# Optimization experiments

Hardware: AMD Instinct MI355X
Metric: run time of the kernel (lower is better)

## Reference

```python
import jax, jax.numpy as jnp
import numpy as np

V, PV, D, H, NC = 100000, 50, 128, 128, 2
L, B = 512, 64


def setup_inputs() -> dict:
    key = jax.random.key(0)
    ks = jax.random.split(key, 20)
    s = 0.05
    x = jax.random.randint(ks[0], (L, B), 0, V)
    y = jax.random.randint(ks[1], (B,), 0, 2)
    p = jax.random.randint(ks[2], (L, B), 0, PV)
    # pack_padded_sequence requires descending lengths
    lengths = jnp.sort(jax.random.randint(ks[3], (B,), 1, L + 1))[::-1]
    idx = jnp.arange(L, dtype=jnp.int32)
    left_child = jnp.broadcast_to(idx - 1, (B, L))  # left-deep chain; -1 => no child
    right_child = jnp.full((B, L), -1, dtype=jnp.int32)
    return dict(
        x=x, y=y, p=p, lengths=lengths,
        left_child=left_child, right_child=right_child,
        embed=jax.random.normal(ks[4], (V, D)) * s,
        Wih_f=jax.random.normal(ks[5], (4 * H, D)) * s,
        Whh_f=jax.random.normal(ks[6], (4 * H, H)) * s,
        b_f=jnp.zeros((4 * H,)),
        Wih_b=jax.random.normal(ks[7], (4 * H, D)) * s,
        Whh_b=jax.random.normal(ks[8], (4 * H, H)) * s,
        b_b=jnp.zeros((4 * H,)),
        Wiou=jax.random.normal(ks[9], (D, 3 * H)) * s,
        Uiou=jax.random.normal(ks[10], (H, 3 * H)) * s,
        biou=jnp.zeros((3 * H,)),
        Wf=jax.random.normal(ks[11], (D, H)) * s,
        Uf=jax.random.normal(ks[12], (H, H)) * s,
        bf=jnp.zeros((H,)),
        Wout=jax.random.normal(ks[13], (NC, 2 * H)) * s,
        bout=jnp.zeros((NC,)),
        w1=jnp.ones(()),
        w2=jnp.ones(()),
    )


def _lstm_dir(emb, mask, Wih, Whh, b, reverse):
    # length-masked uni-directional LSTM (emulates packed sequence); PyTorch gate order i,f,g,o
    Bm = emb.shape[1]
    def step(carry, inp):
        h, c = carry
        xt, m = inp  # [B,D], [B,1]
        g = xt @ Wih.T + h @ Whh.T + b
        i, f, gg, o = jnp.split(g, 4, axis=-1)
        cn = jax.nn.sigmoid(f) * c + jax.nn.sigmoid(i) * jnp.tanh(gg)
        hn = jax.nn.sigmoid(o) * jnp.tanh(cn)
        return (jnp.where(m, hn, h), jnp.where(m, cn, c)), None
    init = (jnp.zeros((Bm, H), emb.dtype), jnp.zeros((Bm, H), emb.dtype))
    (hT, _cT), _ = jax.lax.scan(step, init, (emb, mask), reverse=reverse)
    return hT  # final hidden [B,H]


def _tree_lstm(emb_k, length, left, right, Wiou, Uiou, biou, Wf, Uf, bf):
    # child-sum binary tree LSTM over one sample; nodes in topological order
    x_iou = emb_k @ Wiou + biou  # [L,3H]
    x_f = emb_k @ Wf + bf        # [L,H]
    def step(carry, inp):
        h_all, c_all = carry
        j, li, ri = inp
        def child(ix):
            v = (ix >= 0).astype(emb_k.dtype)
            ixc = jnp.maximum(ix, 0)
            return h_all[ixc] * v, c_all[ixc] * v
        hl, cl = child(li)
        hr, cr = child(ri)
        iou = x_iou[j] + (hl + hr) @ Uiou
        i, o, u = jnp.split(iou, 3)
        fl = jax.nn.sigmoid(x_f[j] + hl @ Uf)
        fr = jax.nn.sigmoid(x_f[j] + hr @ Uf)
        c = jax.nn.sigmoid(i) * jnp.tanh(u) + fl * cl + fr * cr
        h = jax.nn.sigmoid(o) * jnp.tanh(c)
        return (h_all.at[j].set(h), c_all.at[j].set(c)), None
    init = (jnp.zeros((L, H), emb_k.dtype), jnp.zeros((L, H), emb_k.dtype))
    (h_all, c_all), _ = jax.lax.scan(
        step, init, (jnp.arange(L, dtype=jnp.int32), left, right))
    root = length - 1  # last valid node is the root of the chain
    return c_all[root], h_all[root]


def reference(x, y, p, lengths, left_child, right_child, embed,
              Wih_f, Whh_f, b_f, Wih_b, Whh_b, b_b,
              Wiou, Uiou, biou, Wf, Uf, bf, Wout, bout, w1, w2):
    emb = embed[x]  # [L,B,D]; dropout layers treated as identity (eval)
    mask = (jnp.arange(L)[:, None] < lengths[None, :])[:, :, None]
    sent_vec = _lstm_dir(emb, mask, Wih_f, Whh_f, b_f, False)  # hidden[0][0], [B,H]
    _hb = _lstm_dir(emb, mask, Wih_b, Whh_b, b_b, True)        # bwd dir (unused downstream)
    emb_b = jnp.transpose(emb, (1, 0, 2))  # [B,L,D]
    t_state, t_hidden = jax.vmap(
        lambda e, ln, l, r: _tree_lstm(e, ln, l, r, Wiou, Uiou, biou, Wf, Uf, bf)
    )(emb_b, lengths, left_child, right_child)  # [B,H] each
    t_hidden = w1 * t_hidden + w2 * sent_vec    # learned mix of tree root hidden & sentence vec
    tree_out = jnp.concatenate([t_state, t_hidden], axis=1)  # [B,2H]
    pred = jax.nn.sigmoid(tree_out @ Wout.T + bout)           # [B,2]
    true = jax.nn.one_hot(jnp.clip(y, 0, 1), NC, dtype=pred.dtype)
    pc = jnp.clip(pred, 1e-7, 1.0 - 1e-7)
    loss = -jnp.mean(true * jnp.log(pc) + (1.0 - true) * jnp.log(1.0 - pc))
    return loss
```

## Files before the change

kernel.cpp:

```cpp
#include <hip/hip_runtime.h>

typedef unsigned short u16;
typedef __attribute__((ext_vector_type(8))) short bf16x8;
typedef __attribute__((ext_vector_type(4))) float f32x4;

#define LSEQ 512
#define BN   64
#define DD   128
#define HH   128
#define CHUNK 64


__device__ __forceinline__ u16 f2b(float f) {
  union { float f; unsigned i; } v; v.f = f;
  unsigned i = v.i;
  return (u16)((i + 0x7fffu + ((i >> 16) & 1u)) >> 16);
}
__device__ __forceinline__ unsigned cvt_pk_bf16(float lo, float hi) {
  unsigned r;
  asm("v_cvt_pk_bf16_f32 %0, %1, %2" : "=v"(r) : "v"(lo), "v"(hi));
  return r;
}
__device__ __forceinline__ float rcpf(float x) {
  return __builtin_amdgcn_rcpf(x);
}
__device__ __forceinline__ float sigm(float x) {
  return rcpf(1.f + __expf(-x));
}
__device__ __forceinline__ float tanh_f(float x) {
  x = fminf(15.f, fmaxf(-15.f, x));
  float e = __expf(2.f * x);
  return (e - 1.f) * rcpf(e + 1.f);
}


__global__ __launch_bounds__(512, 1) void eiou_kernel(
    const int* __restrict__ x, const int* __restrict__ lengths,
    const float* __restrict__ embed,
    const float* __restrict__ Wih_f, const float* __restrict__ b_f,
    const float* __restrict__ Wiou, const float* __restrict__ biou,
    const float* __restrict__ Wf, const float* __restrict__ bfv,
    float* __restrict__ xfwd, float* __restrict__ xtree) {
  const int bid = blockIdx.x;
  const int b = bid & (BN - 1);
  const bool tree = (bid >> 6) & 1;
  const int c0 = (bid >> 7) * CHUNK;
  int len = lengths[b];
  len = (len < 1) ? 1 : (len > LSEQ ? LSEQ : len);
  if (c0 >= len) return;

  const int tid = threadIdx.x;
  const int w = tid >> 6, l = tid & 63, lr = l & 15, lq = l >> 4;
  const int d = w * 16 + lr;

  __shared__ __align__(16) u16 echunk[CHUNK * 128];
  __shared__ int toks_s[CHUNK];

  bf16x8 bfragE[4][4];
  if (!tree) {
#pragma unroll
    for (int g = 0; g < 4; g++) {
      const int n = g * 128 + w * 16 + lr;
#pragma unroll
      for (int ks = 0; ks < 4; ks++) {
        const int k0 = ks * 32 + lq * 8;
        float4 lo = *(const float4*)(Wih_f + n * 128 + k0);
        float4 hi = *(const float4*)(Wih_f + n * 128 + k0 + 4);
        bf16x8 fr;
        fr[0] = (short)f2b(lo.x); fr[1] = (short)f2b(lo.y);
        fr[2] = (short)f2b(lo.z); fr[3] = (short)f2b(lo.w);
        fr[4] = (short)f2b(hi.x); fr[5] = (short)f2b(hi.y);
        fr[6] = (short)f2b(hi.z); fr[7] = (short)f2b(hi.w);
        bfragE[g][ks] = fr;
      }
    }
  } else {
#pragma unroll
    for (int g = 0; g < 4; g++) {
      const int col = (g < 3) ? (g * 128 + w * 16 + lr) : (w * 16 + lr);
#pragma unroll
      for (int ks = 0; ks < 4; ks++) {
        const int k0 = ks * 32 + lq * 8;
        bf16x8 fe;
#pragma unroll
        for (int j = 0; j < 8; j++) {
          const int k = k0 + j;
          float ve = (g < 3) ? Wiou[k * 384 + col] : Wf[k * 128 + col];
          fe[j] = (short)f2b(ve);
        }
        bfragE[g][ks] = fe;
      }
    }
  }

  float bias0, bias1, bias2, bias3;
  if (!tree) {
    bias0 = b_f[d];        bias1 = b_f[128 + d];
    bias2 = b_f[256 + d];  bias3 = b_f[384 + d];
  } else {
    bias0 = biou[d];       bias1 = biou[128 + d];
    bias2 = biou[256 + d]; bias3 = bfv[d];
  }

  if (tid < CHUNK) {
    int i = c0 + tid;
    int tt = (i < len) ? i : (len - 1);
    toks_s[tid] = x[tt * BN + b];
  }
  __syncthreads();

#pragma unroll
  for (int j = 0; j < 4; j++) {
    int u = tid + j * 512;
    int r = u >> 5;
    int c4 = (u & 31) * 4;
    int row = toks_s[r];
    float4 v = *(const float4*)(embed + (size_t)row * DD + c4);
    unsigned p01 = cvt_pk_bf16(v.x, v.y);
    unsigned p23 = cvt_pk_bf16(v.z, v.w);
    unsigned long long packed =
        (unsigned long long)p01 | ((unsigned long long)p23 << 32);
    int bo = (r * 256 + c4 * 2) ^ ((r & 7) << 4);
    *(unsigned long long*)((char*)echunk + bo) = packed;
  }
  __syncthreads();

  float* const gbase = (tree ? xtree : xfwd) + (size_t)b * (LSEQ * 512);
  const f32x4 zf = (f32x4){0.f, 0.f, 0.f, 0.f};

  for (int t0 = 0; t0 < CHUNK; t0 += 16) {
    const int rb = t0 + lr;
    bf16x8 ae[4];
#pragma unroll
    for (int ks = 0; ks < 4; ks++) {
      int bo = (rb * 256 + ks * 64 + lq * 16) ^ ((rb & 7) << 4);
      ae[ks] = *(const bf16x8*)((const char*)echunk + bo);
    }
    f32x4 EBv[4];
#pragma unroll
    for (int g = 0; g < 4; g++)
      EBv[g] = __builtin_amdgcn_mfma_f32_16x16x32_bf16(ae[0], bfragE[g][0],
                                                       zf, 0, 0, 0);
#pragma unroll
    for (int ks = 1; ks < 4; ks++)
#pragma unroll
      for (int g = 0; g < 4; g++)
        EBv[g] = __builtin_amdgcn_mfma_f32_16x16x32_bf16(
            ae[ks], bfragE[g][ks], EBv[g], 0, 0, 0);
#pragma unroll
    for (int rg = 0; rg < 4; rg++) {
      float4 wv = {EBv[0][rg] + bias0, EBv[1][rg] + bias1,
                   EBv[2][rg] + bias2, EBv[3][rg] + bias3};
      *(float4*)(gbase +
                 ((size_t)(c0 + t0 + lq * 4 + rg) * 512 + d * 4)) = wv;
    }
  }
}

__global__ __launch_bounds__(512, 1) void chains_fast(
    const int* __restrict__ lengths,
    const float* __restrict__ Whh_f,
    const float* __restrict__ Uiou, const float* __restrict__ Uf,
    const float* __restrict__ xfwd, const float* __restrict__ xtree,
    float* __restrict__ sent_vec, float* __restrict__ t_state,
    float* __restrict__ t_hidden) {
  const bool tree = blockIdx.x >= BN;
  const int b = blockIdx.x & (BN - 1);
  int len = lengths[b];
  len = (len < 1) ? 1 : (len > LSEQ ? LSEQ : len);
  const int tid = threadIdx.x;
  const int w = tid >> 6, l = tid & 63, lr = l & 15, lq = l >> 4;
  const int d = w * 16 + lr;

  __shared__ __align__(16) u16 aK[2][128];

  bf16x8 bfragH[4][4];
  if (!tree) {
#pragma unroll
    for (int g = 0; g < 4; g++) {
      const int n = g * 128 + w * 16 + lr;
#pragma unroll
      for (int ks = 0; ks < 4; ks++) {
        const int k0 = ks * 32 + lq * 8;
        float4 lo = *(const float4*)(Whh_f + n * 128 + k0);
        float4 hi = *(const float4*)(Whh_f + n * 128 + k0 + 4);
        bf16x8 fr;
        fr[0] = (short)f2b(lo.x); fr[1] = (short)f2b(lo.y);
        fr[2] = (short)f2b(lo.z); fr[3] = (short)f2b(lo.w);
        fr[4] = (short)f2b(hi.x); fr[5] = (short)f2b(hi.y);
        fr[6] = (short)f2b(hi.z); fr[7] = (short)f2b(hi.w);
        bfragH[g][ks] = fr;
      }
    }
  } else {
#pragma unroll
    for (int g = 0; g < 4; g++) {
      const int col = (g < 3) ? (g * 128 + w * 16 + lr) : (w * 16 + lr);
#pragma unroll
      for (int ks = 0; ks < 4; ks++) {
        const int k0 = ks * 32 + lq * 8;
        bf16x8 fh;
#pragma unroll
        for (int j = 0; j < 8; j++) {
          const int k = k0 + j;
          float vh = (g < 3) ? Uiou[k * 384 + col] : Uf[k * 128 + col];
          fh[j] = (short)f2b(vh);
        }
        bfragH[g][ks] = fh;
      }
    }
  }

  if (tid < HH) { aK[0][tid] = 0; aK[1][tid] = 0; }

  const char* const ak_rd = (const char*)aK + (lq << 4);
  u16* const ak_wr = &aK[0][0] + d;

  const float* const xbase =
      (tree ? xtree : xfwd) + (size_t)b * (LSEQ * 512) + (size_t)d * 4;

  const f32x4 zf = (f32x4){0.f, 0.f, 0.f, 0.f};
  float c = 0.f, h = 0.f;
  int t = 0;

  float4 ev_e = *(const float4*)(xbase + 0 * 512);
  float4 ev_o = *(const float4*)(xbase + 1 * 512);

  __syncthreads();

#define STEPF(PAR, EVREG)                                                     \
  {                                                                           \
    bf16x8 ah[4];                                                             \
    _Pragma("unroll")                                                         \
    for (int ks = 0; ks < 4; ks++)                                            \
      ah[ks] = *(const bf16x8*)(ak_rd + (PAR) * 256 + ks * 64);               \
    float4 evn = *(const float4*)(xbase + (size_t)(t + 2) * 512);             \
    f32x4 accA[4], accB[4], accC[4], accD[4];                                 \
    _Pragma("unroll")                                                         \
    for (int g = 0; g < 4; g++) {                                             \
      accA[g] = __builtin_amdgcn_mfma_f32_16x16x32_bf16(ah[0], bfragH[g][0],  \
                                                        zf, 0, 0, 0);         \
      accB[g] = __builtin_amdgcn_mfma_f32_16x16x32_bf16(ah[1], bfragH[g][1],  \
                                                        zf, 0, 0, 0);         \
      accC[g] = __builtin_amdgcn_mfma_f32_16x16x32_bf16(ah[2], bfragH[g][2],  \
                                                        zf, 0, 0, 0);         \
      accD[g] = __builtin_amdgcn_mfma_f32_16x16x32_bf16(ah[3], bfragH[g][3],  \
                                                        zf, 0, 0, 0);         \
    }                                                                         \
    float g0 = (accA[0][0] + accB[0][0]) + (accC[0][0] + accD[0][0]) +        \
               (EVREG).x;                                                     \
    float g1 = (accA[1][0] + accB[1][0]) + (accC[1][0] + accD[1][0]) +        \
               (EVREG).y;                                                     \
    float g2 = (accA[2][0] + accB[2][0]) + (accC[2][0] + accD[2][0]) +        \
               (EVREG).z;                                                     \
    float g3 = (accA[3][0] + accB[3][0]) + (accC[3][0] + accD[3][0]) +        \
               (EVREG).w;                                                     \
    if (!tree) {                                                              \
      float ii = sigm(g0), ff = sigm(g1), gg = tanh_f(g2), oo = sigm(g3);     \
      c = ff * c + ii * gg;                                                   \
      h = oo * tanh_f(c);                                                     \
    } else {                                                                  \
      float ii = sigm(g0), oo = sigm(g1), uu = tanh_f(g2), fl = sigm(g3);     \
      c = ii * uu + fl * c;                                                   \
      h = oo * tanh_f(c);                                                     \
    }                                                                         \
    unsigned hp = cvt_pk_bf16(h, h);                                          \
    if (l < 16) ak_wr[((PAR) ^ 1) * 128] = (u16)hp;                           \
    (EVREG) = evn;                                                            \
    asm volatile("s_waitcnt lgkmcnt(0)" ::: "memory");                        \
    __builtin_amdgcn_s_barrier();                                             \
    __builtin_amdgcn_sched_barrier(0);                                        \
    t++;                                                                      \
  }

  while (t + 2 <= len) {
    STEPF(0, ev_e)
    STEPF(1, ev_o)
  }
  if (t < len) {
    STEPF(0, ev_e)
  }
#undef STEPF

  if (l < 16) {
    if (!tree) {
      sent_vec[b * HH + d] = h;
    } else {
      t_state[b * HH + d] = c;
      t_hidden[b * HH + d] = h;
    }
  }
}

__global__ __launch_bounds__(512, 1) void chains_kernel(
    const int* __restrict__ x, const int* __restrict__ lengths,
    const float* __restrict__ embed,
    const float* __restrict__ Wih_f, const float* __restrict__ Whh_f,
    const float* __restrict__ b_f,
    const float* __restrict__ Wiou, const float* __restrict__ Uiou,
    const float* __restrict__ biou,
    const float* __restrict__ Wf, const float* __restrict__ Uf,
    const float* __restrict__ bfv,
    float* __restrict__ sent_vec, float* __restrict__ t_state,
    float* __restrict__ t_hidden) {
  const bool tree = blockIdx.x >= BN;
  const int b = blockIdx.x & (BN - 1);
  int len = lengths[b];
  len = (len < 1) ? 1 : (len > LSEQ ? LSEQ : len);
  const int tid = threadIdx.x;
  const int w = tid >> 6, l = tid & 63, lr = l & 15, lq = l >> 4;
  const int d = w * 16 + lr;

  __shared__ __align__(16) u16 echunk[CHUNK * 128];
  __shared__ __align__(16) float estage[8 * 16 * 16 * 4];
  __shared__ __align__(16) u16 aK[2][128];
  __shared__ int toks[LSEQ];

  bf16x8 bfragH[4][4], bfragE[4][4];
  if (!tree) {
#pragma unroll
    for (int g = 0; g < 4; g++) {
      const int n = g * 128 + w * 16 + lr;
#pragma unroll
      for (int ks = 0; ks < 4; ks++) {
        const int k0 = ks * 32 + lq * 8;
        {
          float4 lo = *(const float4*)(Whh_f + n * 128 + k0);
          float4 hi = *(const float4*)(Whh_f + n * 128 + k0 + 4);
          bf16x8 fr;
          fr[0] = (short)f2b(lo.x); fr[1] = (short)f2b(lo.y);
          fr[2] = (short)f2b(lo.z); fr[3] = (short)f2b(lo.w);
          fr[4] = (short)f2b(hi.x); fr[5] = (short)f2b(hi.y);
          fr[6] = (short)f2b(hi.z); fr[7] = (short)f2b(hi.w);
          bfragH[g][ks] = fr;
        }
        {
          float4 lo = *(const float4*)(Wih_f + n * 128 + k0);
          float4 hi = *(const float4*)(Wih_f + n * 128 + k0 + 4);
          bf16x8 fr;
          fr[0] = (short)f2b(lo.x); fr[1] = (short)f2b(lo.y);
          fr[2] = (short)f2b(lo.z); fr[3] = (short)f2b(lo.w);
          fr[4] = (short)f2b(hi.x); fr[5] = (short)f2b(hi.y);
          fr[6] = (short)f2b(hi.z); fr[7] = (short)f2b(hi.w);
          bfragE[g][ks] = fr;
        }
      }
    }
  } else {
#pragma unroll
    for (int g = 0; g < 4; g++) {
      const int col = (g < 3) ? (g * 128 + w * 16 + lr) : (w * 16 + lr);
#pragma unroll
      for (int ks = 0; ks < 4; ks++) {
        const int k0 = ks * 32 + lq * 8;
        bf16x8 fh, fe;
#pragma unroll
        for (int j = 0; j < 8; j++) {
          const int k = k0 + j;
          float vh, ve;
          if (g < 3) { vh = Uiou[k * 384 + col]; ve = Wiou[k * 384 + col]; }
          else       { vh = Uf[k * 128 + col];   ve = Wf[k * 128 + col]; }
          fh[j] = (short)f2b(vh);
          fe[j] = (short)f2b(ve);
        }
        bfragH[g][ks] = fh;
        bfragE[g][ks] = fe;
      }
    }
  }

  float bias0, bias1, bias2, bias3;
  if (!tree) {
    bias0 = b_f[d];        bias1 = b_f[128 + d];
    bias2 = b_f[256 + d];  bias3 = b_f[384 + d];
  } else {
    bias0 = biou[d];       bias1 = biou[128 + d];
    bias2 = biou[256 + d]; bias3 = bfv[d];
  }

  for (int i = tid; i < LSEQ; i += 512) {
    int tt = (i < len) ? i : (len - 1);
    toks[i] = x[tt * BN + b];
  }
  if (tid < HH) { aK[0][tid] = 0; aK[1][tid] = 0; }

  char* const es_base = (char*)estage;
  const int erd = (w << 12) + (lr << 4);
  const int ewr = (w << 12) + (lq << 10) + (lr << 4);
  const char* const ak_rd = (const char*)aK + (lq << 4);
  u16* const ak_wr = &aK[0][0] + d;

  const f32x4 zf = (f32x4){0.f, 0.f, 0.f, 0.f};
  float c = 0.f, h = 0.f;
  int t = 0;

#define EBATCH(T0)                                                            \
  {                                                                           \
    const int rb = ((T0) & (CHUNK - 1)) + lr;                                 \
    bf16x8 ae[4];                                                             \
    _Pragma("unroll")                                                         \
    for (int ks = 0; ks < 4; ks++) {                                          \
      int bo = (rb * 256 + ks * 64 + lq * 16) ^ ((rb & 7) << 4);              \
      ae[ks] = *(const bf16x8*)((const char*)echunk + bo);                    \
    }                                                                         \
    f32x4 EBv[4];                                                             \
    _Pragma("unroll")                                                         \
    for (int g = 0; g < 4; g++)                                               \
      EBv[g] = __builtin_amdgcn_mfma_f32_16x16x32_bf16(ae[0], bfragE[g][0],   \
                                                       zf, 0, 0, 0);          \
    _Pragma("unroll")                                                         \
    for (int ks = 1; ks < 4; ks++)                                            \
      _Pragma("unroll")                                                       \
      for (int g = 0; g < 4; g++)                                             \
        EBv[g] = __builtin_amdgcn_mfma_f32_16x16x32_bf16(                     \
            ae[ks], bfragE[g][ks], EBv[g], 0, 0, 0);                          \
    _Pragma("unroll")                                                         \
    for (int rg = 0; rg < 4; rg++) {                                          \
      f32x4 wv = {EBv[0][rg] + bias0, EBv[1][rg] + bias1,                     \
                  EBv[2][rg] + bias2, EBv[3][rg] + bias3};                    \
      *(f32x4*)(es_base + ewr + rg * 256) = wv;                               \
    }                                                                         \
  }

#define STEPB(S)                                                              \
  {                                                                           \
    bf16x8 ah[4];                                                             \
    _Pragma("unroll")                                                         \
    for (int ks = 0; ks < 4; ks++)                                            \
      ah[ks] = *(const bf16x8*)(ak_rd + ((S) & 1) * 256 + ks * 64);           \
    f32x4 ev = *(const f32x4*)(es_base + erd + (S) * 256);                    \
    f32x4 accA[4], accB[4];                                                   \
    _Pragma("unroll")                                                         \
    for (int g = 0; g < 4; g++) {                                             \
      accA[g] = __builtin_amdgcn_mfma_f32_16x16x32_bf16(ah[0], bfragH[g][0],  \
                                                        zf, 0, 0, 0);         \
      accB[g] = __builtin_amdgcn_mfma_f32_16x16x32_bf16(ah[2], bfragH[g][2],  \
                                                        zf, 0, 0, 0);         \
    }                                                                         \
    _Pragma("unroll")                                                         \
    for (int g = 0; g < 4; g++) {                                             \
      accA[g] = __builtin_amdgcn_mfma_f32_16x16x32_bf16(                      \
          ah[1], bfragH[g][1], accA[g], 0, 0, 0);                             \
      accB[g] = __builtin_amdgcn_mfma_f32_16x16x32_bf16(                      \
          ah[3], bfragH[g][3], accB[g], 0, 0, 0);                             \
    }                                                                         \
    float g0 = accA[0][0] + accB[0][0] + ev[0];                               \
    float g1 = accA[1][0] + accB[1][0] + ev[1];                               \
    float g2 = accA[2][0] + accB[2][0] + ev[2];                               \
    float g3 = accA[3][0] + accB[3][0] + ev[3];                               \
    if (!tree) {                                                              \
      float ii = sigm(g0), ff = sigm(g1), gg = tanh_f(g2), oo = sigm(g3);     \
      c = ff * c + ii * gg;                                                   \
      h = oo * tanh_f(c);                                                     \
    } else {                                                                  \
      float ii = sigm(g0), oo = sigm(g1), uu = tanh_f(g2), fl = sigm(g3);     \
      c = ii * uu + fl * c;                                                   \
      h = oo * tanh_f(c);                                                     \
    }                                                                         \
    unsigned hp = cvt_pk_bf16(h, h);                                          \
    if (l < 16) ak_wr[(((S) & 1) ^ 1) * 128] = (u16)hp;                       \
    __syncthreads();                                                          \
  }

#define STEPT(S) if (tb + (S) < tend) STEPB(S)

  for (int c0 = 0; c0 < len; c0 += CHUNK) {
    __syncthreads();
#pragma unroll
    for (int j = 0; j < 4; j++) {
      int u = tid + j * 512;
      int r = u >> 5;
      int c4 = (u & 31) * 4;
      int row = toks[c0 + r];
      float4 v = *(const float4*)(embed + (size_t)row * DD + c4);
      unsigned p01 = cvt_pk_bf16(v.x, v.y);
      unsigned p23 = cvt_pk_bf16(v.z, v.w);
      unsigned long long packed =
          (unsigned long long)p01 | ((unsigned long long)p23 << 32);
      int bo = (r * 256 + c4 * 2) ^ ((r & 7) << 4);
      *(unsigned long long*)((char*)echunk + bo) = packed;
    }
    __syncthreads();

    const int tend = (c0 + CHUNK < len) ? c0 + CHUNK : len;
    while (t + 16 <= tend) {
      EBATCH(t)
      STEPB(0)  STEPB(1)  STEPB(2)  STEPB(3)
      STEPB(4)  STEPB(5)  STEPB(6)  STEPB(7)
      STEPB(8)  STEPB(9)  STEPB(10) STEPB(11)
      STEPB(12) STEPB(13) STEPB(14) STEPB(15)
      t += 16;
    }
    if (t < tend) {
      const int tb = t;
      EBATCH(tb)
      STEPT(0)  STEPT(1)  STEPT(2)  STEPT(3)
      STEPT(4)  STEPT(5)  STEPT(6)  STEPT(7)
      STEPT(8)  STEPT(9)  STEPT(10) STEPT(11)
      STEPT(12) STEPT(13) STEPT(14)
      t = tend;
    }
  }
#undef STEPT
#undef STEPB
#undef EBATCH

  if (l < 16) {
    if (!tree) {
      sent_vec[b * HH + d] = h;
    } else {
      t_state[b * HH + d] = c;
      t_hidden[b * HH + d] = h;
    }
  }
}

__global__ __launch_bounds__(128) void final_kernel(
    const int* __restrict__ y, const float* __restrict__ sent_vec,
    const float* __restrict__ t_state, const float* __restrict__ t_hidden,
    const float* __restrict__ Wout, const float* __restrict__ bout,
    const float* __restrict__ w1, const float* __restrict__ w2,
    float* __restrict__ out) {
  int tid = threadIdx.x;
  int b = tid >> 1, cls = tid & 1;
  float W1 = w1[0], W2 = w2[0];
  const float* wrow = Wout + cls * 256;
  float acc = bout[cls];
  for (int j = 0; j < HH; j++)
    acc += t_state[b * HH + j] * wrow[j];
  for (int j = 0; j < HH; j++)
    acc += (W1 * t_hidden[b * HH + j] + W2 * sent_vec[b * HH + j]) * wrow[128 + j];
  float p = 1.f / (1.f + __expf(-acc));
  p = fminf(1.f - 1e-7f, fmaxf(1e-7f, p));
  int yy = y[b]; yy = yy < 0 ? 0 : (yy > 1 ? 1 : yy);
  float term = (cls == yy) ? __logf(p) : __logf(1.f - p);
  __shared__ float red[128];
  red[tid] = term;
  __syncthreads();
  for (int s = 64; s > 0; s >>= 1) {
    if (tid < s) red[tid] += red[tid + s];
    __syncthreads();
  }
  if (tid == 0) out[0] = -red[0] / 128.f;
}

extern "C" void kernel_launch(void* const* d_in, const int* in_sizes, int n_in,
                              void* d_out, int out_size, void* d_ws, size_t ws_size,
                              hipStream_t stream) {
  (void)in_sizes; (void)n_in; (void)out_size;
  const int*   x       = (const int*)d_in[0];
  const int*   y       = (const int*)d_in[1];
  const int*   lengths = (const int*)d_in[3];
  const float* embed   = (const float*)d_in[6];
  const float* Wih_f   = (const float*)d_in[7];
  const float* Whh_f   = (const float*)d_in[8];
  const float* b_f     = (const float*)d_in[9];
  const float* Wiou    = (const float*)d_in[13];
  const float* Uiou    = (const float*)d_in[14];
  const float* biou    = (const float*)d_in[15];
  const float* Wf      = (const float*)d_in[16];
  const float* Uf      = (const float*)d_in[17];
  const float* bfv     = (const float*)d_in[18];
  const float* Wout    = (const float*)d_in[19];
  const float* bout    = (const float*)d_in[20];
  const float* w1      = (const float*)d_in[21];
  const float* w2      = (const float*)d_in[22];

  float* sent_vec = (float*)d_ws;
  float* t_state  = sent_vec + BN * HH;
  float* t_hidden = t_state + BN * HH;
  const size_t out_bytes = (size_t)BN * HH * 3 * sizeof(float);
  const size_t x4_bytes  = (size_t)BN * LSEQ * 512 * sizeof(float);
  const size_t need = out_bytes + 2 * x4_bytes + (1u << 20);

  if (ws_size >= need) {
    float* xfwd  = (float*)((char*)d_ws + out_bytes);
    float* xtree = xfwd + (size_t)BN * LSEQ * 512;
    eiou_kernel<<<1024, 512, 0, stream>>>(x, lengths, embed, Wih_f, b_f,
                                          Wiou, biou, Wf, bfv, xfwd, xtree);
    chains_fast<<<128, 512, 0, stream>>>(lengths, Whh_f, Uiou, Uf,
                                         xfwd, xtree,
                                         sent_vec, t_state, t_hidden);
  } else {
    chains_kernel<<<128, 512, 0, stream>>>(x, lengths, embed,
                                           Wih_f, Whh_f, b_f,
                                           Wiou, Uiou, biou, Wf, Uf, bfv,
                                           sent_vec, t_state, t_hidden);
  }
  final_kernel<<<1, 128, 0, stream>>>(y, sent_vec, t_state, t_hidden,
                                      Wout, bout, w1, w2, (float*)d_out);
}
```

Before: 402.2 us.

## Halve recurrent-chain block to 4 waves, each covering 32 hidden units

The recurrent chain kernel now runs 256 threads per block instead of 512. Each wave computes two 16-column hidden slices, keeping twice as many bf16 weight fragments in registers and chaining the K-steps through one accumulator rather than summing four partial accumulators. The aim is to cut the per-step barrier cost across fewer waves and drop the extra adds, at the price of twice the MFMA and gate work per wave and higher register pressure. The custom waitcnt plus s_barrier is also replaced by a plain __syncthreads.

```diff
diff --git a/kernel.cpp b/kernel.cpp
--- a/kernel.cpp
+++ b/kernel.cpp
@@ -157,7 +157,7 @@
   }
 }
 
-__global__ __launch_bounds__(512, 1) void chains_fast(
+__global__ __launch_bounds__(256, 1) void chains_fast(
     const int* __restrict__ lengths,
     const float* __restrict__ Whh_f,
     const float* __restrict__ Uiou, const float* __restrict__ Uf,
@@ -170,124 +170,137 @@
   len = (len < 1) ? 1 : (len > LSEQ ? LSEQ : len);
   const int tid = threadIdx.x;
   const int w = tid >> 6, l = tid & 63, lr = l & 15, lq = l >> 4;
-  const int d = w * 16 + lr;
+  const int d0 = w * 32 + lr;
 
   __shared__ __align__(16) u16 aK[2][128];
 
-  bf16x8 bfragH[4][4];
+  bf16x8 bfragH[4][2][4];
   if (!tree) {
 #pragma unroll
-    for (int g = 0; g < 4; g++) {
-      const int n = g * 128 + w * 16 + lr;
-#pragma unroll
-      for (int ks = 0; ks < 4; ks++) {
-        const int k0 = ks * 32 + lq * 8;
-        float4 lo = *(const float4*)(Whh_f + n * 128 + k0);
-        float4 hi = *(const float4*)(Whh_f + n * 128 + k0 + 4);
-        bf16x8 fr;
-        fr[0] = (short)f2b(lo.x); fr[1] = (short)f2b(lo.y);
-        fr[2] = (short)f2b(lo.z); fr[3] = (short)f2b(lo.w);
-        fr[4] = (short)f2b(hi.x); fr[5] = (short)f2b(hi.y);
-        fr[6] = (short)f2b(hi.z); fr[7] = (short)f2b(hi.w);
-        bfragH[g][ks] = fr;
+    for (int g = 0; g < 4; g++)
+#pragma unroll
+      for (int hh = 0; hh < 2; hh++) {
+        const int n = g * 128 + w * 32 + hh * 16 + lr;
+#pragma unroll
+        for (int ks = 0; ks < 4; ks++) {
+          const int k0 = ks * 32 + lq * 8;
+          float4 lo = *(const float4*)(Whh_f + n * 128 + k0);
+          float4 hi = *(const float4*)(Whh_f + n * 128 + k0 + 4);
+          bf16x8 fr;
+          fr[0] = (short)f2b(lo.x); fr[1] = (short)f2b(lo.y);
+          fr[2] = (short)f2b(lo.z); fr[3] = (short)f2b(lo.w);
+          fr[4] = (short)f2b(hi.x); fr[5] = (short)f2b(hi.y);
+          fr[6] = (short)f2b(hi.z); fr[7] = (short)f2b(hi.w);
+          bfragH[g][hh][ks] = fr;
+        }
       }
-    }
   } else {
 #pragma unroll
-    for (int g = 0; g < 4; g++) {
-      const int col = (g < 3) ? (g * 128 + w * 16 + lr) : (w * 16 + lr);
-#pragma unroll
-      for (int ks = 0; ks < 4; ks++) {
-        const int k0 = ks * 32 + lq * 8;
-        bf16x8 fh;
-#pragma unroll
-        for (int j = 0; j < 8; j++) {
-          const int k = k0 + j;
-          float vh = (g < 3) ? Uiou[k * 384 + col] : Uf[k * 128 + col];
-          fh[j] = (short)f2b(vh);
+    for (int g = 0; g < 4; g++)
+#pragma unroll
+      for (int hh = 0; hh < 2; hh++) {
+        const int dcol = w * 32 + hh * 16 + lr;
+#pragma unroll
+        for (int ks = 0; ks < 4; ks++) {
+          const int k0 = ks * 32 + lq * 8;
+          bf16x8 fh;
+#pragma unroll
+          for (int j = 0; j < 8; j++) {
+            const int k = k0 + j;
+            float vh = (g < 3) ? Uiou[k * 384 + g * 128 + dcol]
+                               : Uf[k * 128 + dcol];
+            fh[j] = (short)f2b(vh);
+          }
+          bfragH[g][hh][ks] = fh;
         }
-        bfragH[g][ks] = fh;
       }
-    }
   }
 
   if (tid < HH) { aK[0][tid] = 0; aK[1][tid] = 0; }
 
   const char* const ak_rd = (const char*)aK + (lq << 4);
-  u16* const ak_wr = &aK[0][0] + d;
+  u16* const ak_wr = &aK[0][w * 32 + (l & 31)];
 
   const float* const xbase =
-      (tree ? xtree : xfwd) + (size_t)b * (LSEQ * 512) + (size_t)d * 4;
+      (tree ? xtree : xfwd) + (size_t)b * (LSEQ * 512) + (size_t)d0 * 4;
 
   const f32x4 zf = (f32x4){0.f, 0.f, 0.f, 0.f};
-  float c = 0.f, h = 0.f;
+  float c0v = 0.f, h0v = 0.f, c1v = 0.f, h1v = 0.f;
   int t = 0;
 
-  float4 ev_e = *(const float4*)(xbase + 0 * 512);
-  float4 ev_o = *(const float4*)(xbase + 1 * 512);
+  float4 evA_e = *(const float4*)(xbase + 0 * 512);
+  float4 evB_e = *(const float4*)(xbase + 0 * 512 + 64);
+  float4 evA_o = *(const float4*)(xbase + 1 * 512);
+  float4 evB_o = *(const float4*)(xbase + 1 * 512 + 64);
 
   __syncthreads();
 
-#define STEPF(PAR, EVREG)                                                     \
+#define STEPF(PAR, EVA, EVB)                                                  \
   {                                                                           \
     bf16x8 ah[4];                                                             \
     _Pragma("unroll")                                                         \
     for (int ks = 0; ks < 4; ks++)                                            \
       ah[ks] = *(const bf16x8*)(ak_rd + (PAR) * 256 + ks * 64);               \
-    float4 evn = *(const float4*)(xbase + (size_t)(t + 2) * 512);             \
-    f32x4 accA[4], accB[4], accC[4], accD[4];                                 \
-    _Pragma("unroll")                                                         \
-    for (int g = 0; g < 4; g++) {                                             \
-      accA[g] = __builtin_amdgcn_mfma_f32_16x16x32_bf16(ah[0], bfragH[g][0],  \
-                                                        zf, 0, 0, 0);         \
-      accB[g] = __builtin_amdgcn_mfma_f32_16x16x32_bf16(ah[1], bfragH[g][1],  \
-                                                        zf, 0, 0, 0);         \
-      accC[g] = __builtin_amdgcn_mfma_f32_16x16x32_bf16(ah[2], bfragH[g][2],  \
-                                                        zf, 0, 0, 0);         \
-      accD[g] = __builtin_amdgcn_mfma_f32_16x16x32_bf16(ah[3], bfragH[g][3],  \
-                                                        zf, 0, 0, 0);         \
+    float4 evnA = *(const float4*)(xbase + (size_t)(t + 2) * 512);            \
+    float4 evnB = *(const float4*)(xbase + (size_t)(t + 2) * 512 + 64);       \
+    f32x4 acc[4][2];                                                          \
+    _Pragma("unroll")                                                         \
+    for (int g = 0; g < 4; g++)                                               \
+      _Pragma("unroll")                                                       \
+      for (int hh = 0; hh < 2; hh++)                                          \
+        acc[g][hh] = __builtin_amdgcn_mfma_f32_16x16x32_bf16(                 \
+            ah[0], bfragH[g][hh][0], zf, 0, 0, 0);                            \
+    _Pragma("unroll")                                                         \
+    for (int ks = 1; ks < 4; ks++)                                            \
+      _Pragma("unroll")                                                       \
+      for (int g = 0; g < 4; g++)                                             \
+        _Pragma("unroll")                                                     \
+        for (int hh = 0; hh < 2; hh++)                                        \
+          acc[g][hh] = __builtin_amdgcn_mfma_f32_16x16x32_bf16(               \
+              ah[ks], bfragH[g][hh][ks], acc[g][hh], 0, 0, 0);                \
+    float gA0 = acc[0][0][0] + (EVA).x;                                       \
+    float gA1 = acc[1][0][0] + (EVA).y;                                       \
+    float gA2 = acc[2][0][0] + (EVA).z;                                       \
+    float gA3 = acc[3][0][0] + (EVA).w;                                       \
+    float gB0 = acc[0][1][0] + (EVB).x;                                       \
+    float gB1 = acc[1][1][0] + (EVB).y;                                       \
+    float gB2 = acc[2][1][0] + (EVB).z;                                       \
+    float gB3 = acc[3][1][0] + (EVB).w;                                       \
+    if (!tree) {                                                              \
+      float iA = sigm(gA0), fA = sigm(gA1), gA = tanh_f(gA2), oA = sigm(gA3); \
+      c0v = fA * c0v + iA * gA;  h0v = oA * tanh_f(c0v);                      \
+      float iB = sigm(gB0), fB = sigm(gB1), gB = tanh_f(gB2), oB = sigm(gB3); \
+      c1v = fB * c1v + iB * gB;  h1v = oB * tanh_f(c1v);                      \
+    } else {                                                                  \
+      float iA = sigm(gA0), oA = sigm(gA1), uA = tanh_f(gA2), fA = sigm(gA3); \
+      c0v = iA * uA + fA * c0v;  h0v = oA * tanh_f(c0v);                      \
+      float iB = sigm(gB0), oB = sigm(gB1), uB = tanh_f(gB2), fB = sigm(gB3); \
+      c1v = iB * uB + fB * c1v;  h1v = oB * tanh_f(c1v);                      \
     }                                                                         \
-    float g0 = (accA[0][0] + accB[0][0]) + (accC[0][0] + accD[0][0]) +        \
-               (EVREG).x;                                                     \
-    float g1 = (accA[1][0] + accB[1][0]) + (accC[1][0] + accD[1][0]) +        \
-               (EVREG).y;                                                     \
-    float g2 = (accA[2][0] + accB[2][0]) + (accC[2][0] + accD[2][0]) +        \
-               (EVREG).z;                                                     \
-    float g3 = (accA[3][0] + accB[3][0]) + (accC[3][0] + accD[3][0]) +        \
-               (EVREG).w;                                                     \
-    if (!tree) {                                                              \
-      float ii = sigm(g0), ff = sigm(g1), gg = tanh_f(g2), oo = sigm(g3);     \
-      c = ff * c + ii * gg;                                                   \
-      h = oo * tanh_f(c);                                                     \
-    } else {                                                                  \
-      float ii = sigm(g0), oo = sigm(g1), uu = tanh_f(g2), fl = sigm(g3);     \
-      c = ii * uu + fl * c;                                                   \
-      h = oo * tanh_f(c);                                                     \
-    }                                                                         \
-    unsigned hp = cvt_pk_bf16(h, h);                                          \
-    if (l < 16) ak_wr[((PAR) ^ 1) * 128] = (u16)hp;                           \
-    (EVREG) = evn;                                                            \
-    asm volatile("s_waitcnt lgkmcnt(0)" ::: "memory");                        \
-    __builtin_amdgcn_s_barrier();                                             \
-    __builtin_amdgcn_sched_barrier(0);                                        \
+    unsigned hp = cvt_pk_bf16((l < 16) ? h0v : h1v, 0.f);                     \
+    if (l < 32) ak_wr[((PAR) ^ 1) * 128] = (u16)hp;                           \
+    (EVA) = evnA;                                                             \
+    (EVB) = evnB;                                                             \
+    __syncthreads();                                                          \
     t++;                                                                      \
   }
 
   while (t + 2 <= len) {
-    STEPF(0, ev_e)
-    STEPF(1, ev_o)
+    STEPF(0, evA_e, evB_e)
+    STEPF(1, evA_o, evB_o)
   }
   if (t < len) {
-    STEPF(0, ev_e)
+    STEPF(0, evA_e, evB_e)
   }
 #undef STEPF
 
-  if (l < 16) {
+  if (l < 32) {
+    const int dd = w * 32 + (l & 31);
     if (!tree) {
-      sent_vec[b * HH + d] = h;
+      sent_vec[b * HH + dd] = (l < 16) ? h0v : h1v;
     } else {
-      t_state[b * HH + d] = c;
-      t_hidden[b * HH + d] = h;
+      t_state[b * HH + dd] = (l < 16) ? c0v : c1v;
+      t_hidden[b * HH + dd] = (l < 16) ? h0v : h1v;
     }
   }
 }
@@ -578,7 +591,7 @@
     float* xtree = xfwd + (size_t)BN * LSEQ * 512;
     eiou_kernel<<<1024, 512, 0, stream>>>(x, lengths, embed, Wih_f, b_f,
                                           Wiou, biou, Wf, bfv, xfwd, xtree);
-    chains_fast<<<128, 512, 0, stream>>>(lengths, Whh_f, Uiou, Uf,
+    chains_fast<<<128, 256, 0, stream>>>(lengths, Whh_f, Uiou, Uf,
                                          xfwd, xtree,
                                          sent_vec, t_state, t_hidden);
   } else {
```

Measured after the change: 439.3 us. +9.2%, slower.
